# Performance work log

Hardware: AMD Instinct MI355X
Metric: run time of the kernel (lower is better)

Reference implementation:

```python
import jax, jax.numpy as jnp
import numpy as np

B, S, D, N_CODES = 8, 512, 768, 8921


def setup_inputs() -> dict:
    key = jax.random.key(0)
    k1, k2, k3, k4 = jax.random.split(key, 4)
    chunk_embeddings = jax.random.normal(k1, (B, S, D), dtype=jnp.float32)
    # bool mask over chunks; force first chunk valid so no row is all -inf
    chunk_mask = jax.random.bernoulli(k2, 0.9, (B, S))
    chunk_mask = chunk_mask.at[:, 0].set(True)
    code_queries = jax.random.normal(k3, (N_CODES, D), dtype=jnp.float32) * 0.02
    classification_weights = jax.random.normal(k4, (N_CODES, D), dtype=jnp.float32) * 0.02
    return {
        "chunk_embeddings": chunk_embeddings,
        "chunk_mask": chunk_mask,
        "code_queries": code_queries,
        "classification_weights": classification_weights,
    }


def reference(chunk_embeddings, chunk_mask, code_queries, classification_weights):
    # chunk_embeddings: [B, S, D], chunk_mask: [B, S] bool
    # code_queries / classification_weights: [N, D]
    scale = jnp.asarray(code_queries.shape[-1], chunk_embeddings.dtype) ** 0.5
    # attention_logits: [B, N, S]
    attention_logits = jnp.einsum("nd,bsd->bns", code_queries, chunk_embeddings) / scale
    neg_inf = jnp.asarray(-jnp.inf, attention_logits.dtype)
    attention_logits = jnp.where(chunk_mask[:, None, :], attention_logits, neg_inf)
    attention_weights = jax.nn.softmax(attention_logits, axis=-1)
    # dropout is identity in eval mode
    # code_embeddings: [B, N, D]
    code_embeddings = jnp.einsum("bns,bsd->bnd", attention_weights, chunk_embeddings)
    logits = jnp.einsum("bnd,nd->bn", code_embeddings, classification_weights)
    return logits, attention_weights
```

## Files before the change

### kernel.cpp

```cpp
#include <hip/hip_runtime.h>
#include <hip/hip_bf16.h>
#include <math.h>

typedef __bf16 bf16x8 __attribute__((ext_vector_type(8)));
typedef float f32x4 __attribute__((ext_vector_type(4)));

#define B_DIM 8
#define S_DIM 512
#define D_DIM 768
#define NC 8921
#define N_PAD 8960
#define TILE_N 64
#define N_TILES 140
#define NKCH 24
#define ROWB 64
#define BUFB 32768
#define MASK_BYTES 16384
#define SWZ(a) ((a) ^ ((((unsigned)(a)) >> 3) & 0x30))

typedef const __attribute__((address_space(1))) void* gas1_t;
typedef __attribute__((address_space(3))) void* las3_t;

__global__ void prep_mask_kernel(const unsigned char* __restrict__ raw, float* __restrict__ bias) {
  __shared__ int s_ms, s_f32;
  int tid = threadIdx.x;
  if (tid == 0) { s_ms = 0; s_f32 = 0; }
  __syncthreads();
  int ms = 0, f32c = 0;
  for (int i = tid; i < B_DIM * S_DIM; i += 256) {
    unsigned char c = raw[i];
    if ((i & 3) != 0 && c != 0) ms++;
    if ((i & 3) == 3 && c == 0x3F) f32c++;
  }
  atomicAdd(&s_ms, ms);
  atomicAdd(&s_f32, f32c);
  __syncthreads();
  int mode = (s_ms == 0) ? 0 : ((s_f32 > 500) ? 2 : 1);
  for (int i = tid; i < B_DIM * S_DIM; i += 256) {
    bool m;
    if (mode == 0)      m = ((const int*)raw)[i] != 0;
    else if (mode == 1) m = raw[i] != 0;
    else                m = ((const float*)raw)[i] != 0.0f;
    bias[i] = m ? 0.0f : -INFINITY;
  }
}

__global__ void cvt_kernel(const float* __restrict__ src, __bf16* __restrict__ dst, long nvalid) {
  long i = ((long)blockIdx.x * blockDim.x + threadIdx.x) * 8;
  bf16x8 o;
  if (i + 8 <= nvalid) {
    float4 a = *reinterpret_cast<const float4*>(src + i);
    float4 b = *reinterpret_cast<const float4*>(src + i + 4);
    o[0] = (__bf16)a.x; o[1] = (__bf16)a.y; o[2] = (__bf16)a.z; o[3] = (__bf16)a.w;
    o[4] = (__bf16)b.x; o[5] = (__bf16)b.y; o[6] = (__bf16)b.z; o[7] = (__bf16)b.w;
  } else {
#pragma unroll
    for (int j = 0; j < 8; ++j) o[j] = (__bf16)0.0f;
  }
  *reinterpret_cast<bf16x8*>(dst + i) = o;
}

__launch_bounds__(512, 2)
__global__ void fused_kernel(const __bf16* __restrict__ Eb, const __bf16* __restrict__ Qb,
                             const __bf16* __restrict__ Wb, const float* __restrict__ bias,
                             float* __restrict__ out) {
  __shared__ __attribute__((aligned(16))) char smem[2 * BUFB];

  const int bid = blockIdx.x;
  const int b = bid & 7;
  const int nbase = (bid >> 3) * TILE_N;
  const int tid = threadIdx.x;
  const int lane = tid & 63;
  const int wave = tid >> 6;
  const int wm = wave >> 2;
  const int wsl = wave & 3;
  const int l15 = lane & 15;
  const int lg = lane >> 4;

  f32x4 accL[2][8], accG[2][8];
  f32x4 zero = {0.f, 0.f, 0.f, 0.f};
#pragma unroll
  for (int mt = 0; mt < 2; ++mt)
#pragma unroll
    for (int nt = 0; nt < 8; ++nt) { accL[mt][nt] = zero; accG[mt][nt] = zero; }

  int srcE[4];
#pragma unroll
  for (int j = 0; j < 4; ++j) {
    int phys = (wave * 4 + j) * 1024 + lane * 16;
    int lgo = SWZ(phys);
    srcE[j] = (lgo >> 6) * 1536 + (lgo & 63);
  }
  const char* eSrc = (const char*)Eb + (size_t)b * S_DIM * 1536;

  int eOff[8];
#pragma unroll
  for (int nt = 0; nt < 8; ++nt) {
    int a = (wsl * 128 + nt * 16 + l15) * ROWB + lg * 16;
    eOff[nt] = SWZ(a);
  }

  const char* qRow = (const char*)Qb + (size_t)(nbase + wm * 32 + l15) * 1536 + lg * 16;
  const char* cRow = (const char*)Wb + (size_t)(nbase + wm * 32 + l15) * 1536 + lg * 16;

  bf16x8 qf0c = *(const bf16x8*)(qRow);
  bf16x8 qf1c = *(const bf16x8*)(qRow + 16 * 1536);
  bf16x8 cf0c = *(const bf16x8*)(cRow);
  bf16x8 cf1c = *(const bf16x8*)(cRow + 16 * 1536);
#pragma unroll
  for (int j = 0; j < 4; ++j)
    __builtin_amdgcn_global_load_lds((gas1_t)(eSrc + srcE[j]),
        (las3_t)(smem + (wave * 4 + j) * 1024), 16, 0, 0);
  asm volatile("s_waitcnt vmcnt(0)" ::: "memory");
  __builtin_amdgcn_s_barrier();
  __builtin_amdgcn_sched_barrier(0);

  bf16x8 qf0n, qf1n, cf0n, cf1n;

#define KBODY(T, BUFSEL)                                                              \
  {                                                                                   \
    if ((T) < NKCH - 1) {                                                             \
      const char* qp = qRow + ((T) + 1) * 64;                                         \
      const char* cp = cRow + ((T) + 1) * 64;                                         \
      qf0n = *(const bf16x8*)(qp);                                                    \
      qf1n = *(const bf16x8*)(qp + 16 * 1536);                                        \
      cf0n = *(const bf16x8*)(cp);                                                    \
      cf1n = *(const bf16x8*)(cp + 16 * 1536);                                        \
      const char* es = eSrc + ((T) + 1) * 64;                                         \
      _Pragma("unroll")                                                               \
      for (int j = 0; j < 4; ++j)                                                     \
        __builtin_amdgcn_global_load_lds((gas1_t)(es + srcE[j]),                      \
            (las3_t)(smem + ((BUFSEL) ^ 1) * BUFB + (wave * 4 + j) * 1024), 16, 0, 0);\
      asm volatile("s_waitcnt vmcnt(8)" ::: "memory");                                \
    } else {                                                                          \
      asm volatile("s_waitcnt vmcnt(0)" ::: "memory");                                \
    }                                                                                 \
    __builtin_amdgcn_s_barrier();                                                     \
    __builtin_amdgcn_sched_barrier(0);                                                \
    const char* bufp = smem + (BUFSEL) * BUFB;                                        \
    _Pragma("unroll")                                                                 \
    for (int nt = 0; nt < 8; ++nt) {                                                  \
      bf16x8 bf = *(const bf16x8*)(bufp + eOff[nt]);                                  \
      accL[0][nt] = __builtin_amdgcn_mfma_f32_16x16x32_bf16(qf0c, bf, accL[0][nt], 0, 0, 0); \
      accL[1][nt] = __builtin_amdgcn_mfma_f32_16x16x32_bf16(qf1c, bf, accL[1][nt], 0, 0, 0); \
      accG[0][nt] = __builtin_amdgcn_mfma_f32_16x16x32_bf16(cf0c, bf, accG[0][nt], 0, 0, 0); \
      accG[1][nt] = __builtin_amdgcn_mfma_f32_16x16x32_bf16(cf1c, bf, accG[1][nt], 0, 0, 0); \
    }                                                                                 \
    qf0c = qf0n; qf1c = qf1n; cf0c = cf0n; cf1c = cf1n;                               \
  }

#pragma unroll 1
  for (int tp = 0; tp < NKCH / 2; ++tp) {
    KBODY(tp * 2, 0)
    KBODY(tp * 2 + 1, 1)
  }
#undef KBODY

  __syncthreads();
  float* redA = (float*)smem;
  float* redB = ((float*)smem) + 256;

  const float scale = 0.036084391824351615f;
  const float* brow = bias + b * S_DIM;
  float bval[8];
#pragma unroll
  for (int nt = 0; nt < 8; ++nt) bval[nt] = brow[wsl * 128 + nt * 16 + l15];

  float rmax[2][4];
#pragma unroll
  for (int mt = 0; mt < 2; ++mt)
#pragma unroll
    for (int r = 0; r < 4; ++r) rmax[mt][r] = -INFINITY;

#pragma unroll
  for (int mt = 0; mt < 2; ++mt)
#pragma unroll
    for (int nt = 0; nt < 8; ++nt)
#pragma unroll
      for (int r = 0; r < 4; ++r) {
        float v = accL[mt][nt][r] * scale + bval[nt];
        accL[mt][nt][r] = v;
        rmax[mt][r] = fmaxf(rmax[mt][r], v);
      }

#pragma unroll
  for (int mt = 0; mt < 2; ++mt)
#pragma unroll
    for (int r = 0; r < 4; ++r) {
      float v = rmax[mt][r];
      v = fmaxf(v, __shfl_xor(v, 1));
      v = fmaxf(v, __shfl_xor(v, 2));
      v = fmaxf(v, __shfl_xor(v, 4));
      v = fmaxf(v, __shfl_xor(v, 8));
      rmax[mt][r] = v;
    }
  if (l15 == 0) {
#pragma unroll
    for (int mt = 0; mt < 2; ++mt)
#pragma unroll
      for (int r = 0; r < 4; ++r) redA[wsl * 64 + wm * 32 + mt * 16 + lg * 4 + r] = rmax[mt][r];
  }
  __syncthreads();

  float gmax[2][4];
#pragma unroll
  for (int mt = 0; mt < 2; ++mt)
#pragma unroll
    for (int r = 0; r < 4; ++r) {
      int row = wm * 32 + mt * 16 + lg * 4 + r;
      gmax[mt][r] = fmaxf(fmaxf(redA[row], redA[64 + row]), fmaxf(redA[128 + row], redA[192 + row]));
    }
  __syncthreads();

  float rsum[2][4], pg[2][4];
#pragma unroll
  for (int mt = 0; mt < 2; ++mt)
#pragma unroll
    for (int r = 0; r < 4; ++r) { rsum[mt][r] = 0.f; pg[mt][r] = 0.f; }

#pragma unroll
  for (int mt = 0; mt < 2; ++mt)
#pragma unroll
    for (int nt = 0; nt < 8; ++nt)
#pragma unroll
      for (int r = 0; r < 4; ++r) {
        float p = __expf(accL[mt][nt][r] - gmax[mt][r]);
        accL[mt][nt][r] = p;
        rsum[mt][r] += p;
        pg[mt][r] += p * accG[mt][nt][r];
      }

#pragma unroll
  for (int mt = 0; mt < 2; ++mt)
#pragma unroll
    for (int r = 0; r < 4; ++r) {
      float s1 = rsum[mt][r], s2 = pg[mt][r];
      s1 += __shfl_xor(s1, 1); s1 += __shfl_xor(s1, 2); s1 += __shfl_xor(s1, 4); s1 += __shfl_xor(s1, 8);
      s2 += __shfl_xor(s2, 1); s2 += __shfl_xor(s2, 2); s2 += __shfl_xor(s2, 4); s2 += __shfl_xor(s2, 8);
      rsum[mt][r] = s1; pg[mt][r] = s2;
    }
  if (l15 == 0) {
#pragma unroll
    for (int mt = 0; mt < 2; ++mt)
#pragma unroll
      for (int r = 0; r < 4; ++r) {
        int row = wm * 32 + mt * 16 + lg * 4 + r;
        redA[wsl * 64 + row] = rsum[mt][r];
        redB[wsl * 64 + row] = pg[mt][r];
      }
  }
  __syncthreads();

  float inv[2][4];
#pragma unroll
  for (int mt = 0; mt < 2; ++mt)
#pragma unroll
    for (int r = 0; r < 4; ++r) {
      int row = wm * 32 + mt * 16 + lg * 4 + r;
      float st = redA[row] + redA[64 + row] + redA[128 + row] + redA[192 + row];
      inv[mt][r] = 1.0f / st;
    }

  float* outW = out + (size_t)B_DIM * NC;
#pragma unroll
  for (int mt = 0; mt < 2; ++mt)
#pragma unroll
    for (int r = 0; r < 4; ++r) {
      int gn = nbase + wm * 32 + mt * 16 + lg * 4 + r;
      if (gn < NC) {
        size_t base = ((size_t)b * NC + gn) * S_DIM + wsl * 128 + l15;
        float iv = inv[mt][r];
#pragma unroll
        for (int nt = 0; nt < 8; ++nt) outW[base + nt * 16] = accL[mt][nt][r] * iv;
      }
    }

  if (wsl == 0 && l15 == 0) {
#pragma unroll
    for (int mt = 0; mt < 2; ++mt)
#pragma unroll
      for (int r = 0; r < 4; ++r) {
        int row = wm * 32 + mt * 16 + lg * 4 + r;
        int gn = nbase + row;
        if (gn < NC) {
          float tot = redB[row] + redB[64 + row] + redB[128 + row] + redB[192 + row];
          out[(size_t)b * NC + gn] = tot * inv[mt][r];
        }
      }
  }
}

__launch_bounds__(512, 2)
__global__ void fused_fallback(const float* __restrict__ E32, const float* __restrict__ Q32,
                               const float* __restrict__ W32,
                               const float* __restrict__ bias, float* __restrict__ out) {
  __shared__ __attribute__((aligned(16))) __bf16 sE[S_DIM][40];
  __shared__ __attribute__((aligned(16))) __bf16 sQ[TILE_N][40];
  __shared__ __attribute__((aligned(16))) __bf16 sC[TILE_N][40];
  __shared__ float redA[4][TILE_N];
  __shared__ float redB[4][TILE_N];

  const int bid = blockIdx.x;
  const int b = bid & 7;
  const int nbase = (bid >> 3) * TILE_N;
  const int tid = threadIdx.x;
  const int lane = tid & 63;
  const int wave = tid >> 6;
  const int wm = wave >> 2, wsl = wave & 3;
  const int l15 = lane & 15, lg = lane >> 4;

  f32x4 accL[2][8], accG[2][8];
  f32x4 zero = {0.f, 0.f, 0.f, 0.f};
#pragma unroll
  for (int mt = 0; mt < 2; ++mt)
#pragma unroll
    for (int nt = 0; nt < 8; ++nt) { accL[mt][nt] = zero; accG[mt][nt] = zero; }

  const size_t eBase = (size_t)b * S_DIM * D_DIM;

  for (int kt = 0; kt < NKCH; ++kt) {
    const int k0 = kt * 32;
#pragma unroll
    for (int i = 0; i < 4; ++i) {
      int task = tid + i * 512;
      int s = task >> 2, dg = task & 3;
      const float* sp = E32 + eBase + (size_t)s * D_DIM + k0 + dg * 8;
      float4 a = *reinterpret_cast<const float4*>(sp);
      float4 c = *reinterpret_cast<const float4*>(sp + 4);
      bf16x8 v;
      v[0] = (__bf16)a.x; v[1] = (__bf16)a.y; v[2] = (__bf16)a.z; v[3] = (__bf16)a.w;
      v[4] = (__bf16)c.x; v[5] = (__bf16)c.y; v[6] = (__bf16)c.z; v[7] = (__bf16)c.w;
      *reinterpret_cast<bf16x8*>(&sE[s][dg * 8]) = v;
    }
    {
      int t = tid & 255;
      int r = t >> 2, dg = t & 3;
      int gr = nbase + r;
      bf16x8 v;
      if (gr < NC) {
        const float* sp = ((tid < 256) ? Q32 : W32) + (size_t)gr * D_DIM + k0 + dg * 8;
        float4 a = *reinterpret_cast<const float4*>(sp);
        float4 c = *reinterpret_cast<const float4*>(sp + 4);
        v[0] = (__bf16)a.x; v[1] = (__bf16)a.y; v[2] = (__bf16)a.z; v[3] = (__bf16)a.w;
        v[4] = (__bf16)c.x; v[5] = (__bf16)c.y; v[6] = (__bf16)c.z; v[7] = (__bf16)c.w;
      } else {
#pragma unroll
        for (int j = 0; j < 8; ++j) v[j] = (__bf16)0.0f;
      }
      __bf16* dst = (tid < 256) ? &sQ[r][dg * 8] : &sC[r][dg * 8];
      *reinterpret_cast<bf16x8*>(dst) = v;
    }
    __syncthreads();

    bf16x8 qf0 = *reinterpret_cast<const bf16x8*>(&sQ[wm * 32 + l15][lg * 8]);
    bf16x8 qf1 = *reinterpret_cast<const bf16x8*>(&sQ[wm * 32 + 16 + l15][lg * 8]);
    bf16x8 cf0 = *reinterpret_cast<const bf16x8*>(&sC[wm * 32 + l15][lg * 8]);
    bf16x8 cf1 = *reinterpret_cast<const bf16x8*>(&sC[wm * 32 + 16 + l15][lg * 8]);

#pragma unroll
    for (int nt = 0; nt < 8; ++nt) {
      bf16x8 bf = *reinterpret_cast<const bf16x8*>(&sE[wsl * 128 + nt * 16 + l15][lg * 8]);
      accL[0][nt] = __builtin_amdgcn_mfma_f32_16x16x32_bf16(qf0, bf, accL[0][nt], 0, 0, 0);
      accL[1][nt] = __builtin_amdgcn_mfma_f32_16x16x32_bf16(qf1, bf, accL[1][nt], 0, 0, 0);
      accG[0][nt] = __builtin_amdgcn_mfma_f32_16x16x32_bf16(cf0, bf, accG[0][nt], 0, 0, 0);
      accG[1][nt] = __builtin_amdgcn_mfma_f32_16x16x32_bf16(cf1, bf, accG[1][nt], 0, 0, 0);
    }
    __syncthreads();
  }

  const float scale = 0.036084391824351615f;
  const float* brow = bias + b * S_DIM;
  float bval[8];
#pragma unroll
  for (int nt = 0; nt < 8; ++nt) bval[nt] = brow[wsl * 128 + nt * 16 + l15];

  float rmax[2][4];
#pragma unroll
  for (int mt = 0; mt < 2; ++mt)
#pragma unroll
    for (int r = 0; r < 4; ++r) rmax[mt][r] = -INFINITY;
#pragma unroll
  for (int mt = 0; mt < 2; ++mt)
#pragma unroll
    for (int nt = 0; nt < 8; ++nt)
#pragma unroll
      for (int r = 0; r < 4; ++r) {
        float v = accL[mt][nt][r] * scale + bval[nt];
        accL[mt][nt][r] = v;
        rmax[mt][r] = fmaxf(rmax[mt][r], v);
      }
#pragma unroll
  for (int mt = 0; mt < 2; ++mt)
#pragma unroll
    for (int r = 0; r < 4; ++r) {
      float v = rmax[mt][r];
      v = fmaxf(v, __shfl_xor(v, 1)); v = fmaxf(v, __shfl_xor(v, 2));
      v = fmaxf(v, __shfl_xor(v, 4)); v = fmaxf(v, __shfl_xor(v, 8));
      rmax[mt][r] = v;
    }
  if (l15 == 0) {
#pragma unroll
    for (int mt = 0; mt < 2; ++mt)
#pragma unroll
      for (int r = 0; r < 4; ++r) redA[wsl][wm * 32 + mt * 16 + lg * 4 + r] = rmax[mt][r];
  }
  __syncthreads();
  float gmax[2][4];
#pragma unroll
  for (int mt = 0; mt < 2; ++mt)
#pragma unroll
    for (int r = 0; r < 4; ++r) {
      int row = wm * 32 + mt * 16 + lg * 4 + r;
      gmax[mt][r] = fmaxf(fmaxf(redA[0][row], redA[1][row]), fmaxf(redA[2][row], redA[3][row]));
    }
  __syncthreads();
  float rsum[2][4], pg[2][4];
#pragma unroll
  for (int mt = 0; mt < 2; ++mt)
#pragma unroll
    for (int r = 0; r < 4; ++r) { rsum[mt][r] = 0.f; pg[mt][r] = 0.f; }
#pragma unroll
  for (int mt = 0; mt < 2; ++mt)
#pragma unroll
    for (int nt = 0; nt < 8; ++nt)
#pragma unroll
      for (int r = 0; r < 4; ++r) {
        float p = __expf(accL[mt][nt][r] - gmax[mt][r]);
        accL[mt][nt][r] = p;
        rsum[mt][r] += p;
        pg[mt][r] += p * accG[mt][nt][r];
      }
#pragma unroll
  for (int mt = 0; mt < 2; ++mt)
#pragma unroll
    for (int r = 0; r < 4; ++r) {
      float s1 = rsum[mt][r], s2 = pg[mt][r];
      s1 += __shfl_xor(s1, 1); s1 += __shfl_xor(s1, 2); s1 += __shfl_xor(s1, 4); s1 += __shfl_xor(s1, 8);
      s2 += __shfl_xor(s2, 1); s2 += __shfl_xor(s2, 2); s2 += __shfl_xor(s2, 4); s2 += __shfl_xor(s2, 8);
      rsum[mt][r] = s1; pg[mt][r] = s2;
    }
  if (l15 == 0) {
#pragma unroll
    for (int mt = 0; mt < 2; ++mt)
#pragma unroll
      for (int r = 0; r < 4; ++r) {
        int row = wm * 32 + mt * 16 + lg * 4 + r;
        redA[wsl][row] = rsum[mt][r];
        redB[wsl][row] = pg[mt][r];
      }
  }
  __syncthreads();
  float inv[2][4];
#pragma unroll
  for (int mt = 0; mt < 2; ++mt)
#pragma unroll
    for (int r = 0; r < 4; ++r) {
      int row = wm * 32 + mt * 16 + lg * 4 + r;
      float st = redA[0][row] + redA[1][row] + redA[2][row] + redA[3][row];
      inv[mt][r] = 1.0f / st;
    }
  float* outW = out + (size_t)B_DIM * NC;
#pragma unroll
  for (int mt = 0; mt < 2; ++mt)
#pragma unroll
    for (int r = 0; r < 4; ++r) {
      int gn = nbase + wm * 32 + mt * 16 + lg * 4 + r;
      if (gn < NC) {
        size_t base = ((size_t)b * NC + gn) * S_DIM + wsl * 128 + l15;
        float iv = inv[mt][r];
#pragma unroll
        for (int nt = 0; nt < 8; ++nt) outW[base + nt * 16] = accL[mt][nt][r] * iv;
      }
    }
  if (wsl == 0 && l15 == 0) {
#pragma unroll
    for (int mt = 0; mt < 2; ++mt)
#pragma unroll
      for (int r = 0; r < 4; ++r) {
        int row = wm * 32 + mt * 16 + lg * 4 + r;
        int gn = nbase + row;
        if (gn < NC) {
          float tot = redB[0][row] + redB[1][row] + redB[2][row] + redB[3][row];
          out[(size_t)b * NC + gn] = tot * inv[mt][r];
        }
      }
  }
}

extern "C" void kernel_launch(void* const* d_in, const int* in_sizes, int n_in,
                              void* d_out, int out_size, void* d_ws, size_t ws_size,
                              hipStream_t stream) {
  const float* E32 = (const float*)d_in[0];
  const unsigned char* mraw = (const unsigned char*)d_in[1];
  const float* Q32 = (const float*)d_in[2];
  const float* W32 = (const float*)d_in[3];
  float* out = (float*)d_out;

  char* ws = (char*)d_ws;
  float* bias = (float*)ws;
  __bf16* Eb = (__bf16*)(ws + MASK_BYTES);
  __bf16* Qb = (__bf16*)(ws + MASK_BYTES + (size_t)B_DIM * S_DIM * D_DIM * 2);
  __bf16* Wb = (__bf16*)((char*)Qb + (size_t)N_PAD * D_DIM * 2);
  size_t need = MASK_BYTES + (size_t)B_DIM * S_DIM * D_DIM * 2 + 2 * (size_t)N_PAD * D_DIM * 2;
  int preconv = (ws_size >= need) ? 1 : 0;

  prep_mask_kernel<<<1, 256, 0, stream>>>(mraw, bias);

  if (preconv) {
    long nE = (long)B_DIM * S_DIM * D_DIM;
    cvt_kernel<<<(int)(nE / 8 / 256), 256, 0, stream>>>(E32, Eb, nE);
    long nQ = (long)NC * D_DIM;
    long nQp = (long)N_PAD * D_DIM;
    cvt_kernel<<<(int)(nQp / 8 / 256), 256, 0, stream>>>(Q32, Qb, nQ);
    cvt_kernel<<<(int)(nQp / 8 / 256), 256, 0, stream>>>(W32, Wb, nQ);
    fused_kernel<<<N_TILES * B_DIM, 512, 0, stream>>>(Eb, Qb, Wb, bias, out);
  } else {
    fused_fallback<<<N_TILES * B_DIM, 512, 0, stream>>>(E32, Q32, W32, bias, out);
  }
}
```

Measured before the change: 234.4 us.

## Stage attention-weight output through LDS for coalesced nontemporal 16-byte stores

The attention-weight write-back now transposes each wave's tile through padded shared memory, so lanes emit contiguous 16-byte nontemporal stores per row instead of strided 4-byte scalar stores. This targets the large [B,N,S] output write, which dominates traffic. The 1/sqrt(D) scale is folded into the bf16 conversion of the queries, and the reduction buffers move to their own shared arrays. To make this work, shared memory grows to about 65 KB and an extra barrier is added per k-chunk, which could reduce occupancy or add sync cost. Rounding also changes slightly because the scale is applied before the bf16 cast.

```diff
diff --git a/kernel.cpp b/kernel.cpp
--- a/kernel.cpp
+++ b/kernel.cpp
@@ -45,14 +45,17 @@
   }
 }
 
-__global__ void cvt_kernel(const float* __restrict__ src, __bf16* __restrict__ dst, long nvalid) {
+__global__ void cvt_kernel(const float* __restrict__ src, __bf16* __restrict__ dst,
+                           long nvalid, float scale) {
   long i = ((long)blockIdx.x * blockDim.x + threadIdx.x) * 8;
   bf16x8 o;
   if (i + 8 <= nvalid) {
     float4 a = *reinterpret_cast<const float4*>(src + i);
     float4 b = *reinterpret_cast<const float4*>(src + i + 4);
-    o[0] = (__bf16)a.x; o[1] = (__bf16)a.y; o[2] = (__bf16)a.z; o[3] = (__bf16)a.w;
-    o[4] = (__bf16)b.x; o[5] = (__bf16)b.y; o[6] = (__bf16)b.z; o[7] = (__bf16)b.w;
+    o[0] = (__bf16)(a.x * scale); o[1] = (__bf16)(a.y * scale);
+    o[2] = (__bf16)(a.z * scale); o[3] = (__bf16)(a.w * scale);
+    o[4] = (__bf16)(b.x * scale); o[5] = (__bf16)(b.y * scale);
+    o[6] = (__bf16)(b.z * scale); o[7] = (__bf16)(b.w * scale);
   } else {
 #pragma unroll
     for (int j = 0; j < 8; ++j) o[j] = (__bf16)0.0f;
@@ -64,7 +67,9 @@
 __global__ void fused_kernel(const __bf16* __restrict__ Eb, const __bf16* __restrict__ Qb,
                              const __bf16* __restrict__ Wb, const float* __restrict__ bias,
                              float* __restrict__ out) {
-  __shared__ __attribute__((aligned(16))) char smem[2 * BUFB];
+  __shared__ __attribute__((aligned(16))) char smem[66560];
+  __shared__ float redA[4][TILE_N];
+  __shared__ float redB[4][TILE_N];
 
   const int bid = blockIdx.x;
   const int b = bid & 7;
@@ -76,6 +81,8 @@
   const int wsl = wave & 3;
   const int l15 = lane & 15;
   const int lg = lane >> 4;
+  const int l31 = lane & 31;
+  const int hi = lane >> 5;
 
   f32x4 accL[2][8], accG[2][8];
   f32x4 zero = {0.f, 0.f, 0.f, 0.f};
@@ -146,6 +153,9 @@
       accG[0][nt] = __builtin_amdgcn_mfma_f32_16x16x32_bf16(cf0c, bf, accG[0][nt], 0, 0, 0); \
       accG[1][nt] = __builtin_amdgcn_mfma_f32_16x16x32_bf16(cf1c, bf, accG[1][nt], 0, 0, 0); \
     }                                                                                 \
+    asm volatile("s_waitcnt lgkmcnt(0)" ::: "memory");                                \
+    __builtin_amdgcn_s_barrier();     \
+    __builtin_amdgcn_sched_barrier(0);     \
     qf0c = qf0n; qf1c = qf1n; cf0c = cf0n; cf1c = cf1n;                               \
   }
 
@@ -157,10 +167,7 @@
 #undef KBODY
 
   __syncthreads();
-  float* redA = (float*)smem;
-  float* redB = ((float*)smem) + 256;
-
-  const float scale = 0.036084391824351615f;
+
   const float* brow = bias + b * S_DIM;
   float bval[8];
 #pragma unroll
@@ -178,7 +185,7 @@
     for (int nt = 0; nt < 8; ++nt)
 #pragma unroll
       for (int r = 0; r < 4; ++r) {
-        float v = accL[mt][nt][r] * scale + bval[nt];
+        float v = accL[mt][nt][r] + bval[nt];
         accL[mt][nt][r] = v;
         rmax[mt][r] = fmaxf(rmax[mt][r], v);
       }
@@ -198,7 +205,7 @@
 #pragma unroll
     for (int mt = 0; mt < 2; ++mt)
 #pragma unroll
-      for (int r = 0; r < 4; ++r) redA[wsl * 64 + wm * 32 + mt * 16 + lg * 4 + r] = rmax[mt][r];
+      for (int r = 0; r < 4; ++r) redA[wsl][wm * 32 + mt * 16 + lg * 4 + r] = rmax[mt][r];
   }
   __syncthreads();
 
@@ -208,7 +215,7 @@
 #pragma unroll
     for (int r = 0; r < 4; ++r) {
       int row = wm * 32 + mt * 16 + lg * 4 + r;
-      gmax[mt][r] = fmaxf(fmaxf(redA[row], redA[64 + row]), fmaxf(redA[128 + row], redA[192 + row]));
+      gmax[mt][r] = fmaxf(fmaxf(redA[0][row], redA[1][row]), fmaxf(redA[2][row], redA[3][row]));
     }
   __syncthreads();
 
@@ -245,8 +252,8 @@
 #pragma unroll
       for (int r = 0; r < 4; ++r) {
         int row = wm * 32 + mt * 16 + lg * 4 + r;
-        redA[wsl * 64 + row] = rsum[mt][r];
-        redB[wsl * 64 + row] = pg[mt][r];
+        redA[wsl][row] = rsum[mt][r];
+        redB[wsl][row] = pg[mt][r];
       }
   }
   __syncthreads();
@@ -257,22 +264,8 @@
 #pragma unroll
     for (int r = 0; r < 4; ++r) {
       int row = wm * 32 + mt * 16 + lg * 4 + r;
-      float st = redA[row] + redA[64 + row] + redA[128 + row] + redA[192 + row];
+      float st = redA[0][row] + redA[1][row] + redA[2][row] + redA[3][row];
       inv[mt][r] = 1.0f / st;
-    }
-
-  float* outW = out + (size_t)B_DIM * NC;
-#pragma unroll
-  for (int mt = 0; mt < 2; ++mt)
-#pragma unroll
-    for (int r = 0; r < 4; ++r) {
-      int gn = nbase + wm * 32 + mt * 16 + lg * 4 + r;
-      if (gn < NC) {
-        size_t base = ((size_t)b * NC + gn) * S_DIM + wsl * 128 + l15;
-        float iv = inv[mt][r];
-#pragma unroll
-        for (int nt = 0; nt < 8; ++nt) outW[base + nt * 16] = accL[mt][nt][r] * iv;
-      }
     }
 
   if (wsl == 0 && l15 == 0) {
@@ -283,26 +276,53 @@
         int row = wm * 32 + mt * 16 + lg * 4 + r;
         int gn = nbase + row;
         if (gn < NC) {
-          float tot = redB[row] + redB[64 + row] + redB[128 + row] + redB[192 + row];
+          float tot = redB[0][row] + redB[1][row] + redB[2][row] + redB[3][row];
           out[(size_t)b * NC + gn] = tot * inv[mt][r];
         }
       }
   }
+  __syncthreads();
+
+  float* tp = (float*)smem + wave * 2080;
+  float* outW = out + (size_t)B_DIM * NC;
+#pragma unroll
+  for (int mt = 0; mt < 2; ++mt) {
+#pragma unroll
+    for (int nt = 0; nt < 8; ++nt)
+#pragma unroll
+      for (int r = 0; r < 4; ++r)
+        tp[(lg * 4 + r) * 130 + nt * 16 + l15] = accL[mt][nt][r] * inv[mt][r];
+    asm volatile("s_waitcnt lgkmcnt(0)" ::: "memory");
+    __builtin_amdgcn_sched_barrier(0);
+#pragma unroll
+    for (int i = 0; i < 8; ++i) {
+      f32x4 v = *(const f32x4*)&tp[(2 * i + hi) * 130 + l31 * 4];
+      int gn = nbase + wm * 32 + mt * 16 + 2 * i + hi;
+      if (gn < NC) {
+        f32x4* dst = (f32x4*)&outW[((size_t)b * NC + gn) * S_DIM + wsl * 128 + l31 * 4];
+        __builtin_nontemporal_store(v, dst);
+      }
+    }
+    asm volatile("s_waitcnt lgkmcnt(0)" ::: "memory");
+    __builtin_amdgcn_sched_barrier(0);
+  }
 }
 
+#define FB_TILE 64
+#define FB_TILES 140
 __launch_bounds__(512, 2)
 __global__ void fused_fallback(const float* __restrict__ E32, const float* __restrict__ Q32,
                                const float* __restrict__ W32,
                                const float* __restrict__ bias, float* __restrict__ out) {
   __shared__ __attribute__((aligned(16))) __bf16 sE[S_DIM][40];
-  __shared__ __attribute__((aligned(16))) __bf16 sQ[TILE_N][40];
-  __shared__ __attribute__((aligned(16))) __bf16 sC[TILE_N][40];
-  __shared__ float redA[4][TILE_N];
-  __shared__ float redB[4][TILE_N];
+  __shared__ __attribute__((aligned(16))) __bf16 sQ[FB_TILE][40];
+  __shared__ __attribute__((aligned(16))) __bf16 sC[FB_TILE][40];
+  __shared__ float redA[4][FB_TILE];
+  __shared__ float redB[4][FB_TILE];
 
   const int bid = blockIdx.x;
   const int b = bid & 7;
-  const int nbase = (bid >> 3) * TILE_N;
+  const int nbase = (bid >> 3) * FB_TILE;
   const int tid = threadIdx.x;
   const int lane = tid & 63;
   const int wave = tid >> 6;
@@ -318,7 +338,7 @@
 
   const size_t eBase = (size_t)b * S_DIM * D_DIM;
 
-  for (int kt = 0; kt < NKCH; ++kt) {
+  for (int kt = 0; kt < 24; ++kt) {
     const int k0 = kt * 32;
 #pragma unroll
     for (int i = 0; i < 4; ++i) {
@@ -508,13 +528,13 @@
 
   if (preconv) {
     long nE = (long)B_DIM * S_DIM * D_DIM;
-    cvt_kernel<<<(int)(nE / 8 / 256), 256, 0, stream>>>(E32, Eb, nE);
+    cvt_kernel<<<(int)(nE / 8 / 256), 256, 0, stream>>>(E32, Eb, nE, 1.0f);
     long nQ = (long)NC * D_DIM;
     long nQp = (long)N_PAD * D_DIM;
-    cvt_kernel<<<(int)(nQp / 8 / 256), 256, 0, stream>>>(Q32, Qb, nQ);
-    cvt_kernel<<<(int)(nQp / 8 / 256), 256, 0, stream>>>(W32, Wb, nQ);
+    cvt_kernel<<<(int)(nQp / 8 / 256), 256, 0, stream>>>(Q32, Qb, nQ, 0.036084391824351615f);
+    cvt_kernel<<<(int)(nQp / 8 / 256), 256, 0, stream>>>(W32, Wb, nQ, 1.0f);
     fused_kernel<<<N_TILES * B_DIM, 512, 0, stream>>>(Eb, Qb, Wb, bias, out);
   } else {
-    fused_fallback<<<N_TILES * B_DIM, 512, 0, stream>>>(E32, Q32, W32, bias, out);
+    fused_fallback<<<FB_TILES * B_DIM, 512, 0, stream>>>(E32, Q32, W32, bias, out);
   }
 }
```

After: 296.4 us. 26.5% more time.
